# Optimization experiments

Hardware: AMD Instinct MI355X
Metric: run time of the kernel (lower is better)

## Reference

```python
import jax, jax.numpy as jnp
import numpy as np

N_NODES = 100000


def setup_inputs() -> dict:
    key = jax.random.key(0)
    k1, k2, k3, k4, k5 = jax.random.split(key, 5)
    x = jax.random.normal(k1, (N_NODES, 128), dtype=jnp.float32)
    edge_index = jax.random.randint(k2, (2, 1600000), 0, N_NODES, dtype=jnp.int64)
    # Linear weights stored torch-style: W is [out_features, in_features]
    W_l = jax.random.normal(k3, (128, 128), dtype=jnp.float32) * 0.05
    b_l = jax.random.normal(k4, (128,), dtype=jnp.float32) * 0.05
    W_r = jax.random.normal(k5, (128, 128), dtype=jnp.float32) * 0.05
    return {"x": x, "edge_index": edge_index, "W_l": W_l, "b_l": b_l, "W_r": W_r}


def reference(x, edge_index, W_l, b_l, W_r):
    # x_l = lin_l(x)  -> [N, out]
    x_l = x @ W_l.T + b_l
    src, dst = edge_index[0], edge_index[1]
    # sparse adjacency matmul: mean aggregation of neighbor features into each dst node
    agg = jax.ops.segment_sum(x_l[src], dst, num_segments=N_NODES)  # [N, out]
    deg = jax.ops.segment_sum(jnp.ones_like(src, dtype=x.dtype), dst, num_segments=N_NODES)
    y = agg / jnp.maximum(deg, 1.0)[:, None]
    # root/self transform (no bias) and elementwise add
    out_r = x @ W_r.T
    return y + out_r
```

## Files before the change

### kernel.cpp

```cpp
#include <hip/hip_runtime.h>
#include <hip/hip_bf16.h>

#define N_NODES 100000
#define N_EDGES 1600000
#define FEAT 128
#define NBINS 2048
#define BIN_NODES 49
#define PBLK 250
#define CHUNK (N_EDGES / PBLK)
#define NTBL (NBINS + 1)
#define CSR_MAX 1280
#define PREP_BLOCKS (N_NODES * FEAT / 8 / 512)

typedef __bf16 bf16x8 __attribute__((ext_vector_type(8)));
typedef unsigned short ushort8 __attribute__((ext_vector_type(8)));
typedef float f32x4 __attribute__((ext_vector_type(4)));
typedef float f32x2 __attribute__((ext_vector_type(2)));

__device__ __forceinline__ unsigned short f2bf_bits(float f) {
    unsigned u = __builtin_bit_cast(unsigned, f);
    unsigned r = (u + 0x7fffu + ((u >> 16) & 1u)) >> 16;
    return (unsigned short)r;
}

__global__ __launch_bounds__(512) void preppart_kernel(
    const float* __restrict__ x, unsigned short* __restrict__ xbf,
    unsigned int* __restrict__ x8, const int* __restrict__ ei,
    int* __restrict__ offtbl, int* __restrict__ ebin) {
    __shared__ int h[NBINS];
    __shared__ int wsum[8];
    const int tid = threadIdx.x;

    if (blockIdx.x >= PBLK) {
        int t = (blockIdx.x - PBLK) * 512 + tid;
        float4 a = ((const float4*)x)[t * 2];
        float4 b = ((const float4*)x)[t * 2 + 1];
        ushort8 u;
        u[0] = f2bf_bits(a.x); u[1] = f2bf_bits(a.y);
        u[2] = f2bf_bits(a.z); u[3] = f2bf_bits(a.w);
        u[4] = f2bf_bits(b.x); u[5] = f2bf_bits(b.y);
        u[6] = f2bf_bits(b.z); u[7] = f2bf_bits(b.w);
        ((ushort8*)xbf)[t] = u;
        int w0 = __builtin_amdgcn_cvt_pk_fp8_f32(a.x, a.y, 0, false);
        w0     = __builtin_amdgcn_cvt_pk_fp8_f32(a.z, a.w, w0, true);
        int w1 = __builtin_amdgcn_cvt_pk_fp8_f32(b.x, b.y, 0, false);
        w1     = __builtin_amdgcn_cvt_pk_fp8_f32(b.z, b.w, w1, true);
        uint2 p; p.x = (unsigned)w0; p.y = (unsigned)w1;
        ((uint2*)x8)[t] = p;
        return;
    }

    const int b = blockIdx.x;
    const int lane = tid & 63, wid = tid >> 6;

    for (int i = tid; i < NBINS; i += 512) h[i] = 0;
    __syncthreads();

    const int4* dsts = (const int4*)(ei + N_EDGES + b * CHUNK);
    for (int i = tid; i < CHUNK / 4; i += 512) {
        int4 d = dsts[i];
        atomicAdd(&h[d.x / BIN_NODES], 1);
        atomicAdd(&h[d.y / BIN_NODES], 1);
        atomicAdd(&h[d.z / BIN_NODES], 1);
        atomicAdd(&h[d.w / BIN_NODES], 1);
    }
    __syncthreads();

    const int i0 = tid * 4;
    int v0 = h[i0], v1 = h[i0 + 1], v2 = h[i0 + 2], v3 = h[i0 + 3];
    const int s = v0 + v1 + v2 + v3;
    int incl = s;
    #pragma unroll
    for (int d = 1; d < 64; d <<= 1) {
        int up = __shfl_up(incl, d);
        if (lane >= d) incl += up;
    }
    if (lane == 63) wsum[wid] = incl;
    __syncthreads();
    if (tid == 0) {
        int run = 0;
        #pragma unroll
        for (int i = 0; i < 8; ++i) { int v = wsum[i]; wsum[i] = run; run += v; }
    }
    __syncthreads();
    int run = wsum[wid] + incl - s + b * CHUNK;
    int* otb = offtbl + (size_t)b * NTBL;
    h[i0] = run; otb[i0] = run; run += v0;
    h[i0 + 1] = run; otb[i0 + 1] = run; run += v1;
    h[i0 + 2] = run; otb[i0 + 2] = run; run += v2;
    h[i0 + 3] = run; otb[i0 + 3] = run; run += v3;
    if (tid == 0) otb[NBINS] = (b + 1) * CHUNK;
    __syncthreads();

    const int4* srcs = (const int4*)(ei + b * CHUNK);
    for (int i = tid; i < CHUNK / 4; i += 512) {
        int4 s4 = srcs[i];
        int4 d4 = dsts[i];
        int bin, ln, pos;
        bin = d4.x / BIN_NODES; ln = d4.x - bin * BIN_NODES;
        pos = atomicAdd(&h[bin], 1); ebin[pos] = s4.x | (ln << 17);
        bin = d4.y / BIN_NODES; ln = d4.y - bin * BIN_NODES;
        pos = atomicAdd(&h[bin], 1); ebin[pos] = s4.y | (ln << 17);
        bin = d4.z / BIN_NODES; ln = d4.z - bin * BIN_NODES;
        pos = atomicAdd(&h[bin], 1); ebin[pos] = s4.z | (ln << 17);
        bin = d4.w / BIN_NODES; ln = d4.w - bin * BIN_NODES;
        pos = atomicAdd(&h[bin], 1); ebin[pos] = s4.w | (ln << 17);
    }
}

#define ACC8(v)                                                             \
    {                                                                       \
        acc2[0] += __builtin_amdgcn_cvt_pk_f32_fp8((int)(v).x, false);      \
        acc2[1] += __builtin_amdgcn_cvt_pk_f32_fp8((int)(v).x, true);       \
        acc2[2] += __builtin_amdgcn_cvt_pk_f32_fp8((int)(v).y, false);      \
        acc2[3] += __builtin_amdgcn_cvt_pk_f32_fp8((int)(v).y, true);       \
    }

__global__ __launch_bounds__(256) void agg_kernel(
    const unsigned char* __restrict__ x8, const int* __restrict__ offtbl,
    const int* __restrict__ ebin, unsigned short* __restrict__ xbarbf,
    int* __restrict__ degs) {
    __shared__ int lcnt[BIN_NODES];
    __shared__ int loff[BIN_NODES];
    __shared__ int lcur[BIN_NODES];
    __shared__ int lraw[CSR_MAX];
    __shared__ int lcsr[CSR_MAX];
    __shared__ int wtot[4];

    const int bid = blockIdx.x, tid = threadIdx.x;
    const int b = (bid & 7) * (NBINS / 8) + (bid >> 3);
    int nb = N_NODES - b * BIN_NODES;
    if (nb <= 0) return;
    if (nb > BIN_NODES) nb = BIN_NODES;

    const int lane = tid & 63, wave = tid >> 6;

    int st = 0, L = 0;
    if (tid < PBLK) {
        st = offtbl[(size_t)tid * NTBL + b];
        L  = offtbl[(size_t)tid * NTBL + b + 1] - st;
    }
    if (tid < BIN_NODES) lcnt[tid] = 0;

    int incl = L;
    #pragma unroll
    for (int d = 1; d < 64; d <<= 1) {
        int up = __shfl_up(incl, d);
        if (lane >= d) incl += up;
    }
    if (lane == 63) wtot[wave] = incl;
    __syncthreads();
    int woff = 0;
    #pragma unroll
    for (int w = 0; w < 4; ++w) woff += (w < wave) ? wtot[w] : 0;
    const int pfx = woff + incl - L;

    for (int i = 0; i < L; ++i) {
        int v = ebin[st + i];
        lraw[pfx + i] = v;
        atomicAdd(&lcnt[v >> 17], 1);
    }
    __syncthreads();

    if (wave == 0) {
        int c = (lane < BIN_NODES) ? lcnt[lane] : 0;
        int ic = c;
        #pragma unroll
        for (int d = 1; d < 64; d <<= 1) {
            int up = __shfl_up(ic, d);
            if (lane >= d) ic += up;
        }
        if (lane < BIN_NODES) {
            loff[lane] = ic - c;
            lcur[lane] = ic - c;
        }
    }
    __syncthreads();

    for (int i = 0; i < L; ++i) {
        int v = lraw[pfx + i];
        int pos = atomicAdd(&lcur[v >> 17], 1);
        lcsr[pos] = v & 0x1FFFF;
    }
    __syncthreads();

    const int g = lane >> 4;
    const unsigned c8 = (lane & 15) * 8;
    for (int ln = wave; ln < nb; ln += 4) {
        const int deg = lcnt[ln];
        const int s0 = loff[ln];
        f32x2 acc2[4];
        #pragma unroll
        for (int i = 0; i < 4; ++i) acc2[i] = (f32x2){0.f, 0.f};
        int base = 0;
        const int full16 = deg & ~15;
        for (; base < full16; base += 16) {
            unsigned sA = (unsigned)lcsr[s0 + base + g];
            unsigned sB = (unsigned)lcsr[s0 + base + g + 4];
            unsigned sC = (unsigned)lcsr[s0 + base + g + 8];
            unsigned sD = (unsigned)lcsr[s0 + base + g + 12];
            uint2 va = *(const uint2*)(x8 + ((sA << 7) + c8));
            uint2 vb = *(const uint2*)(x8 + ((sB << 7) + c8));
            uint2 vc = *(const uint2*)(x8 + ((sC << 7) + c8));
            uint2 vd = *(const uint2*)(x8 + ((sD << 7) + c8));
            ACC8(va); ACC8(vb); ACC8(vc); ACC8(vd);
        }
        for (; base < deg; base += 8) {
            int j0 = base + g, j1 = j0 + 4;
            bool pA = j0 < deg, pB = j1 < deg;
            unsigned sA = (unsigned)(pA ? lcsr[s0 + j0] : lcsr[s0]);
            unsigned sB = (unsigned)(pB ? lcsr[s0 + j1] : lcsr[s0]);
            uint2 va = *(const uint2*)(x8 + ((sA << 7) + c8));
            uint2 vb = *(const uint2*)(x8 + ((sB << 7) + c8));
            if (pA) ACC8(va);
            if (pB) ACC8(vb);
        }
        #pragma unroll
        for (int i = 0; i < 4; ++i) {
            #pragma unroll
            for (int k = 0; k < 2; ++k) {
                acc2[i][k] += __shfl_xor(acc2[i][k], 16);
                acc2[i][k] += __shfl_xor(acc2[i][k], 32);
            }
        }
        const int n = b * BIN_NODES + ln;
        if (lane < 16) {
            float inv = 1.0f / (float)(deg > 0 ? deg : 1);
            ushort8 o;
            #pragma unroll
            for (int i = 0; i < 4; ++i) {
                o[2 * i]     = f2bf_bits(acc2[i][0] * inv);
                o[2 * i + 1] = f2bf_bits(acc2[i][1] * inv);
            }
            *(ushort8*)(xbarbf + (size_t)n * FEAT + c8) = o;
        }
        if (lane == 0) degs[n] = deg;
    }
}

__global__ __launch_bounds__(256) void gemm_kernel(
    const unsigned short* __restrict__ xbf, const unsigned short* __restrict__ xbarbf,
    const float* __restrict__ Wl, const float* __restrict__ bl,
    const float* __restrict__ Wr, const int* __restrict__ degs,
    float* __restrict__ out) {

    __shared__ unsigned short lM[32][136];
    __shared__ unsigned short lX[32][136];

    const int tid = threadIdx.x;
    const int wave = tid >> 6, lane = tid & 63;
    const int l15 = lane & 15, lhi = lane >> 4;
    const int colbase = wave * 32;

    bf16x8 bB[2][8];
    float biasv[2];
    #pragma unroll
    for (int ct = 0; ct < 2; ++ct) {
        int col = colbase + ct * 16 + l15;
        biasv[ct] = bl[col];
        const float* wl = Wl + (size_t)col * 128;
        const float* wr = Wr + (size_t)col * 128;
        #pragma unroll
        for (int s = 0; s < 4; ++s) {
            int kb = lhi * 8 + s * 32;
            bf16x8 bfr, cfr;
            #pragma unroll
            for (int i = 0; i < 8; ++i) {
                bfr[i] = __builtin_bit_cast(__bf16, f2bf_bits(wl[kb + i]));
                cfr[i] = __builtin_bit_cast(__bf16, f2bf_bits(wr[kb + i]));
            }
            bB[ct][s] = bfr;
            bB[ct][4 + s] = cfr;
        }
    }

    const int ntiles = N_NODES / 32;
    for (int tile = blockIdx.x; tile < ntiles; tile += gridDim.x) {
        const int row0 = tile * 32;
        {
            int r = tid >> 3;
            int c0 = (tid & 7) * 16;
            const unsigned short* sm = xbarbf + (size_t)(row0 + r) * FEAT + c0;
            const unsigned short* sx = xbf + (size_t)(row0 + r) * FEAT + c0;
            *(ushort8*)&lM[r][c0]     = *(const ushort8*)(sm);
            *(ushort8*)&lM[r][c0 + 8] = *(const ushort8*)(sm + 8);
            *(ushort8*)&lX[r][c0]     = *(const ushort8*)(sx);
            *(ushort8*)&lX[r][c0 + 8] = *(const ushort8*)(sx + 8);
        }
        __syncthreads();

        f32x4 acc[2][2];
        #pragma unroll
        for (int rh = 0; rh < 2; ++rh)
            #pragma unroll
            for (int ct = 0; ct < 2; ++ct) acc[rh][ct] = (f32x4){0.f, 0.f, 0.f, 0.f};

        #pragma unroll
        for (int rh = 0; rh < 2; ++rh) {
            int arow = rh * 16 + l15;
            bf16x8 aM[4], aX[4];
            #pragma unroll
            for (int s = 0; s < 4; ++s) {
                aM[s] = __builtin_bit_cast(bf16x8, *(const ushort8*)&lM[arow][lhi * 8 + s * 32]);
                aX[s] = __builtin_bit_cast(bf16x8, *(const ushort8*)&lX[arow][lhi * 8 + s * 32]);
            }
            #pragma unroll
            for (int ct = 0; ct < 2; ++ct) {
                f32x4 a = acc[rh][ct];
                #pragma unroll
                for (int s = 0; s < 4; ++s)
                    a = __builtin_amdgcn_mfma_f32_16x16x32_bf16(aM[s], bB[ct][s], a, 0, 0, 0);
                #pragma unroll
                for (int s = 0; s < 4; ++s)
                    a = __builtin_amdgcn_mfma_f32_16x16x32_bf16(aX[s], bB[ct][4 + s], a, 0, 0, 0);
                acc[rh][ct] = a;
            }
        }

        #pragma unroll
        for (int rh = 0; rh < 2; ++rh)
            #pragma unroll
            for (int ct = 0; ct < 2; ++ct) {
                int col = colbase + ct * 16 + l15;
                #pragma unroll
                for (int j = 0; j < 4; ++j) {
                    int r = row0 + rh * 16 + lhi * 4 + j;
                    float bias = (degs[r] > 0) ? biasv[ct] : 0.f;
                    out[(size_t)r * FEAT + col] = acc[rh][ct][j] + bias;
                }
            }
        __syncthreads();
    }
}

extern "C" void kernel_launch(void* const* d_in, const int* in_sizes, int n_in,
                              void* d_out, int out_size, void* d_ws, size_t ws_size,
                              hipStream_t stream) {
    const float* x  = (const float*)d_in[0];
    const int*   ei = (const int*)d_in[1];
    const float* Wl = (const float*)d_in[2];
    const float* bl = (const float*)d_in[3];
    const float* Wr = (const float*)d_in[4];
    float* out = (float*)d_out;

    unsigned short* xbf    = (unsigned short*)d_ws;
    unsigned short* xbarbf = xbf + (size_t)N_NODES * FEAT;
    unsigned int* x8       = (unsigned int*)(xbarbf + (size_t)N_NODES * FEAT);
    int* degs   = (int*)(x8 + (size_t)N_NODES * FEAT / 4);
    int* offtbl = degs + N_NODES;
    int* ebin   = offtbl + (size_t)PBLK * NTBL;

    preppart_kernel<<<PBLK + PREP_BLOCKS, 512, 0, stream>>>(x, xbf, x8, ei, offtbl, ebin);
    agg_kernel<<<NBINS, 256, 0, stream>>>((const unsigned char*)x8, offtbl, ebin, xbarbf, degs);
    gemm_kernel<<<1024, 256, 0, stream>>>(xbf, xbarbf, Wl, bl, Wr, degs, out);
}
```

Before: 96.86 us.

## Widen gather loads to 16 bytes and assign contiguous GEMM tiles per XCD

The aggregation kernel now has each lane load 16 fp8 values (uint4) per neighbour row, so 8 lanes cover a row and 8 neighbours are gathered in parallel. Previously 16 lanes each loaded 8 bytes and 4 neighbours were in flight. This cuts the number of load instructions per edge and adds one extra shuffle-reduction stage. The GEMM kernel replaces its grid-stride tile loop with a contiguous range of tiles per XCD, chosen from the block index, to improve L2 locality. That mapping assumes a grid of 1024 blocks (8 XCDs × 128) and the fixed tile count.

```diff
diff --git a/kernel.cpp b/kernel.cpp
--- a/kernel.cpp
+++ b/kernel.cpp
@@ -108,12 +108,16 @@
     }
 }
 
-#define ACC8(v)                                                             \
+#define ACC16(v)                                                            \
     {                                                                       \
         acc2[0] += __builtin_amdgcn_cvt_pk_f32_fp8((int)(v).x, false);      \
         acc2[1] += __builtin_amdgcn_cvt_pk_f32_fp8((int)(v).x, true);       \
         acc2[2] += __builtin_amdgcn_cvt_pk_f32_fp8((int)(v).y, false);      \
         acc2[3] += __builtin_amdgcn_cvt_pk_f32_fp8((int)(v).y, true);       \
+        acc2[4] += __builtin_amdgcn_cvt_pk_f32_fp8((int)(v).z, false);      \
+        acc2[5] += __builtin_amdgcn_cvt_pk_f32_fp8((int)(v).z, true);       \
+        acc2[6] += __builtin_amdgcn_cvt_pk_f32_fp8((int)(v).w, false);      \
+        acc2[7] += __builtin_amdgcn_cvt_pk_f32_fp8((int)(v).w, true);       \
     }
 
 __global__ __launch_bounds__(256) void agg_kernel(
@@ -184,55 +188,53 @@
     }
     __syncthreads();
 
-    const int g = lane >> 4;
-    const unsigned c8 = (lane & 15) * 8;
+    const int g = lane >> 3;
+    const unsigned cb = (lane & 7) * 16;
     for (int ln = wave; ln < nb; ln += 4) {
         const int deg = lcnt[ln];
         const int s0 = loff[ln];
-        f32x2 acc2[4];
-        #pragma unroll
-        for (int i = 0; i < 4; ++i) acc2[i] = (f32x2){0.f, 0.f};
+        f32x2 acc2[8];
+        #pragma unroll
+        for (int i = 0; i < 8; ++i) acc2[i] = (f32x2){0.f, 0.f};
         int base = 0;
         const int full16 = deg & ~15;
         for (; base < full16; base += 16) {
             unsigned sA = (unsigned)lcsr[s0 + base + g];
-            unsigned sB = (unsigned)lcsr[s0 + base + g + 4];
-            unsigned sC = (unsigned)lcsr[s0 + base + g + 8];
-            unsigned sD = (unsigned)lcsr[s0 + base + g + 12];
-            uint2 va = *(const uint2*)(x8 + ((sA << 7) + c8));
-            uint2 vb = *(const uint2*)(x8 + ((sB << 7) + c8));
-            uint2 vc = *(const uint2*)(x8 + ((sC << 7) + c8));
-            uint2 vd = *(const uint2*)(x8 + ((sD << 7) + c8));
-            ACC8(va); ACC8(vb); ACC8(vc); ACC8(vd);
+            unsigned sB = (unsigned)lcsr[s0 + base + 8 + g];
+            uint4 va = *(const uint4*)(x8 + ((sA << 7) + cb));
+            uint4 vb = *(const uint4*)(x8 + ((sB << 7) + cb));
+            ACC16(va); ACC16(vb);
         }
         for (; base < deg; base += 8) {
-            int j0 = base + g, j1 = j0 + 4;
-            bool pA = j0 < deg, pB = j1 < deg;
-            unsigned sA = (unsigned)(pA ? lcsr[s0 + j0] : lcsr[s0]);
-            unsigned sB = (unsigned)(pB ? lcsr[s0 + j1] : lcsr[s0]);
-            uint2 va = *(const uint2*)(x8 + ((sA << 7) + c8));
-            uint2 vb = *(const uint2*)(x8 + ((sB << 7) + c8));
-            if (pA) ACC8(va);
-            if (pB) ACC8(vb);
-        }
-        #pragma unroll
-        for (int i = 0; i < 4; ++i) {
+            int j = base + g;
+            bool p = j < deg;
+            unsigned sv = (unsigned)(p ? lcsr[s0 + j] : lcsr[s0]);
+            uint4 v = *(const uint4*)(x8 + ((sv << 7) + cb));
+            if (p) ACC16(v);
+        }
+        #pragma unroll
+        for (int i = 0; i < 8; ++i) {
             #pragma unroll
             for (int k = 0; k < 2; ++k) {
+                acc2[i][k] += __shfl_xor(acc2[i][k], 8);
                 acc2[i][k] += __shfl_xor(acc2[i][k], 16);
                 acc2[i][k] += __shfl_xor(acc2[i][k], 32);
             }
         }
         const int n = b * BIN_NODES + ln;
-        if (lane < 16) {
+        if (lane < 8) {
             float inv = 1.0f / (float)(deg > 0 ? deg : 1);
-            ushort8 o;
+            ushort8 o0, o1;
             #pragma unroll
             for (int i = 0; i < 4; ++i) {
-                o[2 * i]     = f2bf_bits(acc2[i][0] * inv);
-                o[2 * i + 1] = f2bf_bits(acc2[i][1] * inv);
-            }
-            *(ushort8*)(xbarbf + (size_t)n * FEAT + c8) = o;
+                o0[2 * i]     = f2bf_bits(acc2[i][0] * inv);
+                o0[2 * i + 1] = f2bf_bits(acc2[i][1] * inv);
+                o1[2 * i]     = f2bf_bits(acc2[4 + i][0] * inv);
+                o1[2 * i + 1] = f2bf_bits(acc2[4 + i][1] * inv);
+            }
+            unsigned short* dst = xbarbf + (size_t)n * FEAT + (lane & 7) * 16;
+            *(ushort8*)(dst)     = o0;
+            *(ushort8*)(dst + 8) = o1;
         }
         if (lane == 0) degs[n] = deg;
     }
@@ -274,8 +276,12 @@
         }
     }
 
-    const int ntiles = N_NODES / 32;
-    for (int tile = blockIdx.x; tile < ntiles; tile += gridDim.x) {
+    const int xcd = blockIdx.x & 7;
+    const int sub = blockIdx.x >> 3;
+    const int tile0 = xcd * 390 + (xcd < 5 ? xcd : 5);
+    const int cnt = (xcd < 5) ? 391 : 390;
+    for (int t = sub; t < cnt; t += 128) {
+        const int tile = tile0 + t;
         const int row0 = tile * 32;
         {
             int r = tid >> 3;
```

New measurement: 123.2 us. 27.2% more time.
